# Optimization experiments

Hardware: AMD Instinct MI355X
Metric: run time of the kernel (lower is better)

The kernel has to match this reference:

```python
import jax, jax.numpy as jnp
import numpy as np

B, T, C, H = 2, 2048, 1024, 16
D = C // H  # head_dim = 64

def setup_inputs() -> dict:
    key = jax.random.key(0)
    ks = jax.random.split(key, 5)
    x = jax.random.normal(ks[0], (B, T, C), dtype=jnp.float32)
    # additive causal mask, broadcastable to (B, H, T, T)
    neg = jnp.float32(-1e9)
    causal = jnp.tril(jnp.ones((T, T), dtype=bool))
    attention_mask = jnp.where(causal, 0.0, neg)[None, None, :, :]
    scale = 0.02
    W_attn = jax.random.normal(ks[1], (C, 3 * C), dtype=jnp.float32) * scale
    b_attn = jnp.zeros((3 * C,), dtype=jnp.float32)
    W_proj = jax.random.normal(ks[2], (C, C), dtype=jnp.float32) * scale
    b_proj = jnp.zeros((C,), dtype=jnp.float32)
    return {"x": x, "attention_mask": attention_mask, "W_attn": W_attn,
            "b_attn": b_attn, "W_proj": W_proj, "b_proj": b_proj}

def reference(x, attention_mask, W_attn, b_attn, W_proj, b_proj):
    b, t, c = x.shape
    qkv = x @ W_attn + b_attn                       # (B,T,3C)
    q, k, v = jnp.split(qkv, 3, axis=-1)
    # (B,T,C) -> (B,H,T,D)
    def heads(u):
        return u.reshape(b, t, H, D).transpose(0, 2, 1, 3)
    q, k, v = heads(q), heads(k), heads(v)
    att = jnp.einsum("bhqd,bhkd->bhqk", q, k) * (1.0 / np.sqrt(D))
    att = att + attention_mask
    att_weights = jax.nn.softmax(att, axis=-1)      # (B,H,T,T)
    y = jnp.einsum("bhqk,bhkd->bhqd", att_weights, v)
    y = y.transpose(0, 2, 1, 3).reshape(b, t, c)    # (B,T,C)
    y = y @ W_proj + b_proj
    return (y, att_weights)
```

## Files before the change

kernel.cpp:

```cpp
#include <hip/hip_runtime.h>
#include <hip/hip_bf16.h>

#define B_ 2
#define T_ 2048
#define C_ 1024
#define H_ 16
#define D_ 64
#define BT_ (B_*T_)
#define N3_ (3*C_)
#define NQT_ (T_/64)

typedef float f32x4 __attribute__((ext_vector_type(4)));
typedef unsigned short u16x4 __attribute__((ext_vector_type(4)));
typedef unsigned short u16x8 __attribute__((ext_vector_type(8)));
typedef __bf16 bf16x8 __attribute__((ext_vector_type(8)));

__device__ __forceinline__ f32x4 mfma16(u16x8 a, u16x8 b, f32x4 c) {
  union Cvt { u16x8 u; bf16x8 h; };
  Cvt ua, ub; ua.u = a; ub.u = b;
  return __builtin_amdgcn_mfma_f32_16x16x32_bf16(ua.h, ub.h, c, 0, 0, 0);
}

__device__ __forceinline__ float exp2_fast(float x) {
  return __builtin_amdgcn_exp2f(x);
}

__device__ __forceinline__ unsigned short f2bf(float f) {
  union { float f; unsigned u; } v; v.f = f;
  unsigned r = v.u + 0x7FFFu + ((v.u >> 16) & 1u);
  return (unsigned short)(r >> 16);
}

__device__ __forceinline__ float bf2f(unsigned short u) {
  union { unsigned u; float f; } v; v.u = ((unsigned)u) << 16;
  return v.f;
}

__device__ __forceinline__ void gload_lds16(const unsigned short* g, unsigned short* l) {
  __builtin_amdgcn_global_load_lds(
      (const __attribute__((address_space(1))) unsigned int*)g,
      (__attribute__((address_space(3))) unsigned int*)l, 16, 0, 0);
}

__global__ __launch_bounds__(256) void transpose_to_bf16T(
    const float* __restrict__ W, unsigned short* __restrict__ WT, int K, int N) {
  __shared__ float tile[32][33];
  int n0 = blockIdx.x * 32, k0 = blockIdx.y * 32;
  int tx = threadIdx.x & 31, ty = threadIdx.x >> 5;
#pragma unroll
  for (int i = 0; i < 4; ++i)
    tile[ty + i * 8][tx] = W[(size_t)(k0 + ty + i * 8) * N + n0 + tx];
  __syncthreads();
#pragma unroll
  for (int i = 0; i < 4; ++i)
    WT[(size_t)(n0 + ty + i * 8) * K + k0 + tx] = f2bf(tile[tx][ty + i * 8]);
}

__global__ __launch_bounds__(256) void convert_x(const float* __restrict__ x,
                                                 unsigned short* __restrict__ xb) {
  int i = (blockIdx.x * 256 + threadIdx.x) * 8;
  f32x4 a = *(const f32x4*)(x + i);
  f32x4 b = *(const f32x4*)(x + i + 4);
  u16x8 o;
  o[0]=f2bf(a[0]); o[1]=f2bf(a[1]); o[2]=f2bf(a[2]); o[3]=f2bf(a[3]);
  o[4]=f2bf(b[0]); o[5]=f2bf(b[1]); o[6]=f2bf(b[2]); o[7]=f2bf(b[3]);
  *(u16x8*)(xb + i) = o;
}

__global__ __launch_bounds__(256) void gemm_qkv(
    const unsigned short* __restrict__ xb, const unsigned short* __restrict__ WaT,
    const float* __restrict__ bias, unsigned short* __restrict__ qkv) {
  __shared__ __attribute__((aligned(16))) unsigned short As[128 * 32];
  __shared__ __attribute__((aligned(16))) unsigned short Bs[128 * 32];
  int n0 = blockIdx.x * 128;
  int m0 = blockIdx.y * 128;
  int tid = threadIdx.x;
  int lane = tid & 63, wid = tid >> 6;
  int wm = wid >> 1, wn = wid & 1;
  int l15 = lane & 15, l4 = lane >> 4;
  int srow = lane >> 2, scol = (lane & 3) << 3;

  f32x4 acc[4][4];
#pragma unroll
  for (int i = 0; i < 4; ++i)
#pragma unroll
    for (int j = 0; j < 4; ++j) acc[i][j] = (f32x4){0.f, 0.f, 0.f, 0.f};

  for (int ks = 0; ks < C_ / 32; ++ks) {
#pragma unroll
    for (int j = 0; j < 2; ++j) {
      int row = wid * 16 + j * 64 + srow;
      gload_lds16(xb + (size_t)(m0 + row) * C_ + ks * 32 + scol,
                  &As[(wid * 16 + j * 64) * 32]);
      gload_lds16(WaT + (size_t)(n0 + row) * C_ + ks * 32 + scol,
                  &Bs[(wid * 16 + j * 64) * 32]);
    }
    __syncthreads();
    u16x8 af[4], bfr[4];
#pragma unroll
    for (int mi = 0; mi < 4; ++mi)
      af[mi] = *(const u16x8*)&As[(wm * 64 + mi * 16 + l15) * 32 + l4 * 8];
#pragma unroll
    for (int ni = 0; ni < 4; ++ni)
      bfr[ni] = *(const u16x8*)&Bs[(wn * 64 + ni * 16 + l15) * 32 + l4 * 8];
#pragma unroll
    for (int mi = 0; mi < 4; ++mi)
#pragma unroll
      for (int ni = 0; ni < 4; ++ni) acc[mi][ni] = mfma16(af[mi], bfr[ni], acc[mi][ni]);
    __syncthreads();
  }

  if (n0 < 2 * C_) {
    float qscale = (n0 < C_) ? 0.125f * 1.44269504f : 1.0f;
#pragma unroll
    for (int mi = 0; mi < 4; ++mi)
#pragma unroll
      for (int ni = 0; ni < 4; ++ni)
#pragma unroll
        for (int rr = 0; rr < 4; ++rr) {
          int m = m0 + wm * 64 + mi * 16 + l4 * 4 + rr;
          int n = n0 + wn * 64 + ni * 16 + l15;
          float v = (acc[mi][ni][rr] + bias[n]) * qscale;
          int b = m >> 11, tok = m & (T_ - 1);
          int sect = n >> 10, h = (n >> 6) & 15, d = n & 63;
          size_t idx = ((((size_t)sect * B_ + b) * H_ + h) * T_ + tok) * D_ + d;
          qkv[idx] = f2bf(v);
        }
  } else {
    unsigned short* vbase = qkv + (size_t)2 * B_ * H_ * T_ * D_;
    int m_b = m0 >> 11;
#pragma unroll
    for (int mi = 0; mi < 4; ++mi) {
      int m = m0 + wm * 64 + mi * 16 + l4 * 4;
      int tok = m & (T_ - 1);
#pragma unroll
      for (int ni = 0; ni < 4; ++ni) {
        int n = n0 + wn * 64 + ni * 16 + l15;
        float bi = bias[n];
        int h = (n >> 6) & 15, d = n & 63;
        u16x4 val;
        val[0] = f2bf(acc[mi][ni][0] + bi);
        val[1] = f2bf(acc[mi][ni][1] + bi);
        val[2] = f2bf(acc[mi][ni][2] + bi);
        val[3] = f2bf(acc[mi][ni][3] + bi);
        *(u16x4*)&vbase[(((size_t)m_b * H_ + h) * D_ + d) * T_ + tok] = val;
      }
    }
  }
}

__global__ __launch_bounds__(256) void attn_kernel(
    const unsigned short* __restrict__ qkv, float* __restrict__ att,
    unsigned short* __restrict__ Y) {
  int idx = blockIdx.x;
  int qt = NQT_ - 1 - (idx >> 5);
  int hb = idx & 31;
  int h = hb & 15;
  int b = hb >> 4;
  int q0 = qt * 64;
  int tid = threadIdx.x, lane = tid & 63, wid = tid >> 6;
  int l15 = lane & 15, l4 = lane >> 4;

  const unsigned short* Q = qkv + (((size_t)(0 * B_ + b) * H_ + h) * T_) * D_;
  const unsigned short* K = qkv + (((size_t)(1 * B_ + b) * H_ + h) * T_) * D_;
  const unsigned short* VtG = qkv + (size_t)2 * B_ * H_ * T_ * D_ +
                              (((size_t)b * H_ + h) * D_) * T_;
  float* attbase = att + ((size_t)(b * H_ + h) * T_) * T_;

  __shared__ __attribute__((aligned(16))) unsigned short Ps[2][64][72];
  __shared__ __attribute__((aligned(16))) unsigned short Vt[2][64][72];

  u16x8 qf[2];
#pragma unroll
  for (int c = 0; c < 2; ++c)
    qf[c] = *(const u16x8*)(Q + (size_t)(q0 + wid * 16 + l15) * D_ + c * 32 + l4 * 8);

  int myrow[4];
#pragma unroll
  for (int rr = 0; rr < 4; ++rr) myrow[rr] = q0 + wid * 16 + l4 * 4 + rr;

  float esum[4] = {0.f, 0.f, 0.f, 0.f};
  for (int kt = 0; kt <= qt; ++kt) {
    int k0 = kt * 64;
    f32x4 s[4];
#pragma unroll
    for (int g = 0; g < 4; ++g) s[g] = (f32x4){0.f, 0.f, 0.f, 0.f};
#pragma unroll
    for (int g = 0; g < 4; ++g)
#pragma unroll
      for (int c = 0; c < 2; ++c) {
        u16x8 kf = *(const u16x8*)(K + (size_t)(k0 + g * 16 + l15) * D_ + c * 32 + l4 * 8);
        s[g] = mfma16(qf[c], kf, s[g]);
      }
    if (kt != qt) {
#pragma unroll
      for (int g = 0; g < 4; ++g)
#pragma unroll
        for (int rr = 0; rr < 4; ++rr) esum[rr] += exp2_fast(s[g][rr]);
    } else {
#pragma unroll
      for (int g = 0; g < 4; ++g) {
        int col = k0 + g * 16 + l15;
#pragma unroll
        for (int rr = 0; rr < 4; ++rr)
          esum[rr] += (col > myrow[rr]) ? 0.f : exp2_fast(s[g][rr]);
      }
    }
  }
  float inv_l[4];
#pragma unroll
  for (int rr = 0; rr < 4; ++rr) {
    float e = esum[rr];
    e += __shfl_xor(e, 1);
    e += __shfl_xor(e, 2);
    e += __shfl_xor(e, 4);
    e += __shfl_xor(e, 8);
    inv_l[rr] = 1.f / e;
  }

  f32x4 yacc[4];
#pragma unroll
  for (int g = 0; g < 4; ++g) yacc[g] = (f32x4){0.f, 0.f, 0.f, 0.f};

  for (int kt = 0; kt <= qt; ++kt) {
    int k0 = kt * 64;
    int p = kt & 1;
    {
      int dd = tid >> 2;
      int kq = (tid & 3) * 16;
      const unsigned short* vsrc = VtG + (size_t)dd * T_ + k0 + kq;
      u16x8 v0 = *(const u16x8*)(vsrc);
      u16x8 v1 = *(const u16x8*)(vsrc + 8);
      *(u16x8*)&Vt[p][dd][kq] = v0;
      *(u16x8*)&Vt[p][dd][kq + 8] = v1;
    }
    f32x4 s[4];
#pragma unroll
    for (int g = 0; g < 4; ++g) s[g] = (f32x4){0.f, 0.f, 0.f, 0.f};
#pragma unroll
    for (int g = 0; g < 4; ++g)
#pragma unroll
      for (int c = 0; c < 2; ++c) {
        u16x8 kf = *(const u16x8*)(K + (size_t)(k0 + g * 16 + l15) * D_ + c * 32 + l4 * 8);
        s[g] = mfma16(qf[c], kf, s[g]);
      }
    if (kt != qt) {
#pragma unroll
      for (int g = 0; g < 4; ++g)
#pragma unroll
        for (int rr = 0; rr < 4; ++rr)
          Ps[p][wid * 16 + l4 * 4 + rr][g * 16 + l15] =
              f2bf(exp2_fast(s[g][rr]) * inv_l[rr]);
    } else {
#pragma unroll
      for (int g = 0; g < 4; ++g) {
        int col = k0 + g * 16 + l15;
#pragma unroll
        for (int rr = 0; rr < 4; ++rr) {
          float pv = (col > myrow[rr]) ? 0.f : exp2_fast(s[g][rr]) * inv_l[rr];
          Ps[p][wid * 16 + l4 * 4 + rr][g * 16 + l15] = f2bf(pv);
        }
      }
    }
    {
      int cc = l15 * 4;
#pragma unroll
      for (int jj = 0; jj < 4; ++jj) {
        int rrow = wid * 16 + jj * 4 + l4;
        const unsigned short* ps = &Ps[p][rrow][cc];
        f32x4 o;
        o[0] = bf2f(ps[0]); o[1] = bf2f(ps[1]);
        o[2] = bf2f(ps[2]); o[3] = bf2f(ps[3]);
        *(f32x4*)&attbase[(size_t)(q0 + rrow) * T_ + k0 + cc] = o;
      }
    }
    __syncthreads();
#pragma unroll
    for (int c = 0; c < 2; ++c) {
      u16x8 pf = *(const u16x8*)&Ps[p][wid * 16 + l15][c * 32 + l4 * 8];
#pragma unroll
      for (int g = 0; g < 4; ++g) {
        u16x8 vf = *(const u16x8*)&Vt[p][g * 16 + l15][c * 32 + l4 * 8];
        yacc[g] = mfma16(pf, vf, yacc[g]);
      }
    }
  }

  f32x4 z = (f32x4){0.f, 0.f, 0.f, 0.f};
  for (int kt = qt + 1; kt < NQT_; ++kt) {
    int k0 = kt * 64;
#pragma unroll
    for (int rr = 0; rr < 4; ++rr)
      *(f32x4*)&attbase[(size_t)myrow[rr] * T_ + k0 + l15 * 4] = z;
  }

#pragma unroll
  for (int g = 0; g < 4; ++g)
#pragma unroll
    for (int rr = 0; rr < 4; ++rr)
      Y[(size_t)(b * T_ + myrow[rr]) * C_ + h * D_ + g * 16 + l15] = f2bf(yacc[g][rr]);
}

__global__ __launch_bounds__(256) void gemm_proj(
    const unsigned short* __restrict__ Y, const unsigned short* __restrict__ WpT,
    const float* __restrict__ bias, float* __restrict__ out) {
  __shared__ __attribute__((aligned(16))) unsigned short As[128 * 32];
  __shared__ __attribute__((aligned(16))) unsigned short Bs[128 * 32];
  int n0 = blockIdx.x * 128;
  int m0 = blockIdx.y * 128;
  int tid = threadIdx.x;
  int lane = tid & 63, wid = tid >> 6;
  int wm = wid >> 1, wn = wid & 1;
  int l15 = lane & 15, l4 = lane >> 4;
  int srow = lane >> 2, scol = (lane & 3) << 3;

  f32x4 acc[4][4];
#pragma unroll
  for (int i = 0; i < 4; ++i)
#pragma unroll
    for (int j = 0; j < 4; ++j) acc[i][j] = (f32x4){0.f, 0.f, 0.f, 0.f};

  for (int ks = 0; ks < C_ / 32; ++ks) {
#pragma unroll
    for (int j = 0; j < 2; ++j) {
      int row = wid * 16 + j * 64 + srow;
      gload_lds16(Y + (size_t)(m0 + row) * C_ + ks * 32 + scol,
                  &As[(wid * 16 + j * 64) * 32]);
      gload_lds16(WpT + (size_t)(n0 + row) * C_ + ks * 32 + scol,
                  &Bs[(wid * 16 + j * 64) * 32]);
    }
    __syncthreads();
    u16x8 af[4], bfr[4];
#pragma unroll
    for (int mi = 0; mi < 4; ++mi)
      af[mi] = *(const u16x8*)&As[(wm * 64 + mi * 16 + l15) * 32 + l4 * 8];
#pragma unroll
    for (int ni = 0; ni < 4; ++ni)
      bfr[ni] = *(const u16x8*)&Bs[(wn * 64 + ni * 16 + l15) * 32 + l4 * 8];
#pragma unroll
    for (int mi = 0; mi < 4; ++mi)
#pragma unroll
      for (int ni = 0; ni < 4; ++ni) acc[mi][ni] = mfma16(af[mi], bfr[ni], acc[mi][ni]);
    __syncthreads();
  }
#pragma unroll
  for (int mi = 0; mi < 4; ++mi)
#pragma unroll
    for (int ni = 0; ni < 4; ++ni)
#pragma unroll
      for (int rr = 0; rr < 4; ++rr) {
        int m = m0 + wm * 64 + mi * 16 + l4 * 4 + rr;
        int n = n0 + wn * 64 + ni * 16 + l15;
        out[(size_t)m * C_ + n] = acc[mi][ni][rr] + bias[n];
      }
}

extern "C" void kernel_launch(void* const* d_in, const int* in_sizes, int n_in,
                              void* d_out, int out_size, void* d_ws, size_t ws_size,
                              hipStream_t stream) {
  const float* x = (const float*)d_in[0];
  const float* W_attn = (const float*)d_in[2];
  const float* b_attn = (const float*)d_in[3];
  const float* W_proj = (const float*)d_in[4];
  const float* b_proj = (const float*)d_in[5];

  float* out_y = (float*)d_out;
  float* out_att = (float*)d_out + (size_t)BT_ * C_;

  unsigned short* WaT = (unsigned short*)d_ws;
  unsigned short* WpT = WaT + (size_t)N3_ * C_;
  unsigned short* qkvb = WpT + (size_t)C_ * C_;
  unsigned short* Yb = qkvb + (size_t)3 * B_ * H_ * T_ * D_;
  unsigned short* xb = Yb + (size_t)BT_ * C_;

  transpose_to_bf16T<<<dim3(N3_ / 32, C_ / 32), 256, 0, stream>>>(W_attn, WaT, C_, N3_);
  transpose_to_bf16T<<<dim3(C_ / 32, C_ / 32), 256, 0, stream>>>(W_proj, WpT, C_, C_);
  convert_x<<<dim3(BT_ * C_ / (256 * 8)), 256, 0, stream>>>(x, xb);
  gemm_qkv<<<dim3(N3_ / 128, BT_ / 128), 256, 0, stream>>>(xb, WaT, b_attn, qkvb);
  attn_kernel<<<dim3(NQT_ * H_ * B_), 256, 0, stream>>>(qkvb, out_att, Yb);
  gemm_proj<<<dim3(C_ / 128, BT_ / 128), 256, 0, stream>>>(Yb, WpT, b_proj, out_y);
}
```

Measured before the change: 306.5 us.

## Enlarge attention query tile to 128 rows with 8 waves sharing V tiles

```diff
diff --git a/kernel.cpp b/kernel.cpp
--- a/kernel.cpp
+++ b/kernel.cpp
@@ -8,7 +8,8 @@
 #define D_ 64
 #define BT_ (B_*T_)
 #define N3_ (3*C_)
-#define NQT_ (T_/64)
+#define NKT_ (T_/64)
+#define NQT_ (T_/128)
 
 typedef float f32x4 __attribute__((ext_vector_type(4)));
 typedef unsigned short u16x4 __attribute__((ext_vector_type(4)));
@@ -149,7 +150,7 @@
   }
 }
 
-__global__ __launch_bounds__(256) void attn_kernel(
+__global__ __launch_bounds__(512) void attn_kernel(
     const unsigned short* __restrict__ qkv, float* __restrict__ att,
     unsigned short* __restrict__ Y) {
   int idx = blockIdx.x;
@@ -157,9 +158,11 @@
   int hb = idx & 31;
   int h = hb & 15;
   int b = hb >> 4;
-  int q0 = qt * 64;
+  int q0 = qt * 128;
+  int nkt = 2 * qt + 2;
   int tid = threadIdx.x, lane = tid & 63, wid = tid >> 6;
   int l15 = lane & 15, l4 = lane >> 4;
+  int rowbase = q0 + wid * 16;
 
   const unsigned short* Q = qkv + (((size_t)(0 * B_ + b) * H_ + h) * T_) * D_;
   const unsigned short* K = qkv + (((size_t)(1 * B_ + b) * H_ + h) * T_) * D_;
@@ -167,21 +170,22 @@
                               (((size_t)b * H_ + h) * D_) * T_;
   float* attbase = att + ((size_t)(b * H_ + h) * T_) * T_;
 
-  __shared__ __attribute__((aligned(16))) unsigned short Ps[2][64][72];
+  __shared__ __attribute__((aligned(16))) unsigned short Ps[2][128][72];
   __shared__ __attribute__((aligned(16))) unsigned short Vt[2][64][72];
 
   u16x8 qf[2];
 #pragma unroll
   for (int c = 0; c < 2; ++c)
-    qf[c] = *(const u16x8*)(Q + (size_t)(q0 + wid * 16 + l15) * D_ + c * 32 + l4 * 8);
+    qf[c] = *(const u16x8*)(Q + (size_t)(rowbase + l15) * D_ + c * 32 + l4 * 8);
 
   int myrow[4];
 #pragma unroll
-  for (int rr = 0; rr < 4; ++rr) myrow[rr] = q0 + wid * 16 + l4 * 4 + rr;
+  for (int rr = 0; rr < 4; ++rr) myrow[rr] = rowbase + l4 * 4 + rr;
 
   float esum[4] = {0.f, 0.f, 0.f, 0.f};
-  for (int kt = 0; kt <= qt; ++kt) {
+  for (int kt = 0; kt < nkt; ++kt) {
     int k0 = kt * 64;
+    if (k0 > rowbase + 15) continue;
     f32x4 s[4];
 #pragma unroll
     for (int g = 0; g < 4; ++g) s[g] = (f32x4){0.f, 0.f, 0.f, 0.f};
@@ -192,7 +196,7 @@
         u16x8 kf = *(const u16x8*)(K + (size_t)(k0 + g * 16 + l15) * D_ + c * 32 + l4 * 8);
         s[g] = mfma16(qf[c], kf, s[g]);
       }
-    if (kt != qt) {
+    if (k0 + 63 <= rowbase) {
 #pragma unroll
       for (int g = 0; g < 4; ++g)
 #pragma unroll
@@ -222,43 +226,48 @@
 #pragma unroll
   for (int g = 0; g < 4; ++g) yacc[g] = (f32x4){0.f, 0.f, 0.f, 0.f};
 
-  for (int kt = 0; kt <= qt; ++kt) {
+  for (int kt = 0; kt < nkt; ++kt) {
     int k0 = kt * 64;
     int p = kt & 1;
+    bool wave_masked = (k0 > rowbase + 15);
     {
-      int dd = tid >> 2;
-      int kq = (tid & 3) * 16;
-      const unsigned short* vsrc = VtG + (size_t)dd * T_ + k0 + kq;
-      u16x8 v0 = *(const u16x8*)(vsrc);
-      u16x8 v1 = *(const u16x8*)(vsrc + 8);
-      *(u16x8*)&Vt[p][dd][kq] = v0;
-      *(u16x8*)&Vt[p][dd][kq + 8] = v1;
-    }
-    f32x4 s[4];
-#pragma unroll
-    for (int g = 0; g < 4; ++g) s[g] = (f32x4){0.f, 0.f, 0.f, 0.f};
-#pragma unroll
-    for (int g = 0; g < 4; ++g)
-#pragma unroll
-      for (int c = 0; c < 2; ++c) {
-        u16x8 kf = *(const u16x8*)(K + (size_t)(k0 + g * 16 + l15) * D_ + c * 32 + l4 * 8);
-        s[g] = mfma16(qf[c], kf, s[g]);
-      }
-    if (kt != qt) {
+      int dd = tid >> 3;
+      int kq = (tid & 7) * 8;
+      *(u16x8*)&Vt[p][dd][kq] = *(const u16x8*)(VtG + (size_t)dd * T_ + k0 + kq);
+    }
+    if (wave_masked) {
 #pragma unroll
       for (int g = 0; g < 4; ++g)
 #pragma unroll
         for (int rr = 0; rr < 4; ++rr)
-          Ps[p][wid * 16 + l4 * 4 + rr][g * 16 + l15] =
-              f2bf(exp2_fast(s[g][rr]) * inv_l[rr]);
+          Ps[p][wid * 16 + l4 * 4 + rr][g * 16 + l15] = 0;
     } else {
-#pragma unroll
-      for (int g = 0; g < 4; ++g) {
-        int col = k0 + g * 16 + l15;
-#pragma unroll
-        for (int rr = 0; rr < 4; ++rr) {
-          float pv = (col > myrow[rr]) ? 0.f : exp2_fast(s[g][rr]) * inv_l[rr];
-          Ps[p][wid * 16 + l4 * 4 + rr][g * 16 + l15] = f2bf(pv);
+      f32x4 s[4];
+#pragma unroll
+      for (int g = 0; g < 4; ++g) s[g] = (f32x4){0.f, 0.f, 0.f, 0.f};
+#pragma unroll
+      for (int g = 0; g < 4; ++g)
+#pragma unroll
+        for (int c = 0; c < 2; ++c) {
+          u16x8 kf = *(const u16x8*)(K + (size_t)(k0 + g * 16 + l15) * D_ + c * 32 + l4 * 8);
+          s[g] = mfma16(qf[c], kf, s[g]);
+        }
+      if (k0 + 63 <= rowbase) {
+#pragma unroll
+        for (int g = 0; g < 4; ++g)
+#pragma unroll
+          for (int rr = 0; rr < 4; ++rr)
+            Ps[p][wid * 16 + l4 * 4 + rr][g * 16 + l15] =
+                f2bf(exp2_fast(s[g][rr]) * inv_l[rr]);
+      } else {
+#pragma unroll
+        for (int g = 0; g < 4; ++g) {
+          int col = k0 + g * 16 + l15;
+#pragma unroll
+          for (int rr = 0; rr < 4; ++rr) {
+            float pv = (col > myrow[rr]) ? 0.f : exp2_fast(s[g][rr]) * inv_l[rr];
+            Ps[p][wid * 16 + l4 * 4 + rr][g * 16 + l15] = f2bf(pv);
+          }
         }
       }
     }
@@ -275,19 +284,21 @@
       }
     }
     __syncthreads();
-#pragma unroll
-    for (int c = 0; c < 2; ++c) {
-      u16x8 pf = *(const u16x8*)&Ps[p][wid * 16 + l15][c * 32 + l4 * 8];
-#pragma unroll
-      for (int g = 0; g < 4; ++g) {
-        u16x8 vf = *(const u16x8*)&Vt[p][g * 16 + l15][c * 32 + l4 * 8];
-        yacc[g] = mfma16(pf, vf, yacc[g]);
+    if (!wave_masked) {
+#pragma unroll
+      for (int c = 0; c < 2; ++c) {
+        u16x8 pf = *(const u16x8*)&Ps[p][wid * 16 + l15][c * 32 + l4 * 8];
+#pragma unroll
+        for (int g = 0; g < 4; ++g) {
+          u16x8 vf = *(const u16x8*)&Vt[p][g * 16 + l15][c * 32 + l4 * 8];
+          yacc[g] = mfma16(pf, vf, yacc[g]);
+        }
       }
     }
   }
 
   f32x4 z = (f32x4){0.f, 0.f, 0.f, 0.f};
-  for (int kt = qt + 1; kt < NQT_; ++kt) {
+  for (int kt = nkt; kt < NKT_; ++kt) {
     int k0 = kt * 64;
 #pragma unroll
     for (int rr = 0; rr < 4; ++rr)
@@ -377,6 +388,6 @@
   transpose_to_bf16T<<<dim3(C_ / 32, C_ / 32), 256, 0, stream>>>(W_proj, WpT, C_, C_);
   convert_x<<<dim3(BT_ * C_ / (256 * 8)), 256, 0, stream>>>(x, xb);
   gemm_qkv<<<dim3(N3_ / 128, BT_ / 128), 256, 0, stream>>>(xb, WaT, b_attn, qkvb);
-  attn_kernel<<<dim3(NQT_ * H_ * B_), 256, 0, stream>>>(qkvb, out_att, Yb);
+  attn_kernel<<<dim3(NQT_ * H_ * B_), 512, 0, stream>>>(qkvb, out_att, Yb);
   gemm_proj<<<dim3(C_ / 128, BT_ / 128), 256, 0, stream>>>(Yb, WpT, b_proj, out_y);
 }
```

Result: no change. 311.0 us (+1.5%).
